# Kernel optimization log

Hardware: AMD Instinct MI355X
Metric: run time of the kernel (lower is better)

The kernel has to match this reference:

```python
import jax, jax.numpy as jnp
import numpy as np

B, T, H, D = 4, 2048, 16, 64
HID = H * D
ROPE_THETA = 10000.0


def _rope_tables(t, d, theta):
    # frequencies over half the head dim, duplicated to full head_dim
    inv_freq = 1.0 / (theta ** (np.arange(0, d, 2, dtype=np.float32) / d))  # (d/2,)
    pos = np.arange(t, dtype=np.float32)
    freqs = np.outer(pos, inv_freq)                      # (T, d/2)
    emb = np.concatenate([freqs, freqs], axis=-1)        # (T, d)
    return jnp.asarray(np.cos(emb)), jnp.asarray(np.sin(emb))


def setup_inputs() -> dict:
    key = jax.random.key(0)
    ks = jax.random.split(key, 5)
    s = 1.0 / np.sqrt(HID)
    cos, sin = _rope_tables(T, D, ROPE_THETA)
    return {
        "x": jax.random.normal(ks[0], (B, T, HID), dtype=jnp.float32),
        "cos": cos,
        "sin": sin,
        "wq": jax.random.normal(ks[1], (HID, HID), dtype=jnp.float32) * s,
        "wk": jax.random.normal(ks[2], (HID, HID), dtype=jnp.float32) * s,
        "wv": jax.random.normal(ks[3], (HID, HID), dtype=jnp.float32) * s,
        "wo": jax.random.normal(ks[4], (HID, HID), dtype=jnp.float32) * s,
    }


def _rotate_half(x):
    x1, x2 = jnp.split(x, 2, axis=-1)
    return jnp.concatenate([-x2, x1], axis=-1)


def reference(x, cos, sin, wq, wk, wv, wo):
    b, t, _ = x.shape
    # QKV projections (nn.Linear: y = x @ W^T), reshape to (B, H, T, D)
    q = (x @ wq.T).reshape(b, t, H, D).transpose(0, 2, 1, 3)
    k = (x @ wk.T).reshape(b, t, H, D).transpose(0, 2, 1, 3)
    v = (x @ wv.T).reshape(b, t, H, D).transpose(0, 2, 1, 3)
    # RoPE
    c = cos[None, None, :, :]
    s = sin[None, None, :, :]
    q = q * c + _rotate_half(q) * s
    k = k * c + _rotate_half(k) * s
    # causal SDPA
    scale = 1.0 / jnp.sqrt(jnp.asarray(D, dtype=x.dtype))
    scores = jnp.einsum("bhqd,bhkd->bhqk", q, k) * scale
    causal = jnp.tril(jnp.ones((t, t), dtype=bool))
    scores = jnp.where(causal[None, None], scores, jnp.finfo(scores.dtype).min)
    attn = jax.nn.softmax(scores, axis=-1)
    out = jnp.einsum("bhqk,bhkd->bhqd", attn, v)
    out = out.transpose(0, 2, 1, 3).reshape(b, t, HID)
    return out @ wo.T
```

## Files before the change

### kernel.cpp

```cpp
#include <hip/hip_runtime.h>

#define BSZ 4
#define TT 2048
#define NH 16
#define HD 64
#define HID 1024
#define BT 8192
#define BH 64

typedef unsigned short u16;
typedef unsigned int u32;
typedef unsigned long long u64;
typedef __attribute__((ext_vector_type(4))) float f32x4;
typedef __attribute__((ext_vector_type(8))) short bf16x8;

#define MFMA32(a, b, c) __builtin_amdgcn_mfma_f32_16x16x32_bf16(a, b, c, 0, 0, 0)

typedef const __attribute__((address_space(1))) u32* gp32;
typedef __attribute__((address_space(3))) u32* lp32;

__device__ __forceinline__ u16 f2bf(float f) {
    union { float f; u32 u; } x; x.f = f;
    u32 r = x.u + 0x7FFFu + ((x.u >> 16) & 1u);
    return (u16)(r >> 16);
}

__device__ __forceinline__ void fexp2x4(f32x4& v) {
    float a = v[0], b = v[1], c = v[2], d = v[3];
    asm("v_exp_f32 %0, %0\n\t"
        "v_exp_f32 %1, %1\n\t"
        "v_exp_f32 %2, %2\n\t"
        "v_exp_f32 %3, %3\n\t"
        "s_nop 1"
        : "+v"(a), "+v"(b), "+v"(c), "+v"(d));
    v[0] = a; v[1] = b; v[2] = c; v[3] = d;
}

__global__ __launch_bounds__(256) void cast_kernel(const float* __restrict__ src,
                                                   u16* __restrict__ dst, int n4) {
    int i = blockIdx.x * 256 + threadIdx.x;
    if (i >= n4) return;
    f32x4 v = *(const f32x4*)(src + (size_t)i * 4);
    uint2 u;
    u.x = (u32)f2bf(v[0]) | ((u32)f2bf(v[1]) << 16);
    u.y = (u32)f2bf(v[2]) | ((u32)f2bf(v[3]) << 16);
    *(uint2*)(dst + (size_t)i * 4) = u;
}

__global__ __launch_bounds__(256)
void cast_w_kernel(const float* __restrict__ wq, const float* __restrict__ wk,
                   const float* __restrict__ wv, const float* __restrict__ wo,
                   u16* __restrict__ wqkv, u16* __restrict__ wo_bf) {
    int g = blockIdx.x >> 10;
    int i = (blockIdx.x & 1023) * 256 + threadIdx.x;
    const float* src = (g == 0) ? wq : (g == 1) ? wk : (g == 2) ? wv : wo;
    u16* dst = (g == 3) ? wo_bf : wqkv + (size_t)g * HID * HID;
    f32x4 v = *(const f32x4*)(src + (size_t)i * 4);
    uint2 u;
    u.x = (u32)f2bf(v[0]) | ((u32)f2bf(v[1]) << 16);
    u.y = (u32)f2bf(v[2]) | ((u32)f2bf(v[3]) << 16);
    *(uint2*)(dst + (size_t)i * 4) = u;
}

template<int MODE>
__global__ __launch_bounds__(512, 2)
void gemm_bt(const u16* __restrict__ A, const u16* __restrict__ W,
             float* __restrict__ Cf, u16* __restrict__ qkv, u16* __restrict__ vt,
             const float* __restrict__ cosT, const float* __restrict__ sinT) {
    __shared__ __align__(16) u16 sh[3 * 24576];
    const int tid  = threadIdx.x;
    const int wid  = tid >> 6, lane = tid & 63;
    const int lrow = lane & 15, lk = lane >> 4;
    const int wm   = (wid >> 1) * 64, wn = (wid & 1) * 64;
    const int xcd  = blockIdx.x & 7;
    const int i_   = blockIdx.x >> 3;
    const int mt   = xcd * 4 + (i_ & 3);
    const int nt   = i_ >> 2;
    const int m0   = mt * 256, n0 = nt * 128;

    auto stageA = [&](int buf, int kk, int half) {
        u16* dst = sh + buf * 24576;
        #pragma unroll
        for (int s = 0; s < 2; ++s) {
            int l16 = half * 1024 + s * 512 + tid;
            int r = l16 >> 3, c = l16 & 7;
            int gc = (c ^ (r & 7)) * 8;
            __builtin_amdgcn_global_load_lds(
                (gp32)&A[(size_t)(m0 + r) * HID + kk + gc],
                (lp32)&dst[l16 * 8], 16, 0, 0);
        }
    };
    auto stageB = [&](int buf, int kk) {
        u16* dst = sh + buf * 24576 + 16384;
        #pragma unroll
        for (int s = 0; s < 2; ++s) {
            int l16 = s * 512 + tid;
            int r = l16 >> 3, c = l16 & 7;
            int gc = (c ^ (r & 7)) * 8;
            __builtin_amdgcn_global_load_lds(
                (gp32)&W[(size_t)(n0 + r) * HID + kk + gc],
                (lp32)&dst[l16 * 8], 16, 0, 0);
        }
    };

    f32x4 acc[4][4] = {};

    stageA(0, 0, 0); stageA(0, 0, 1); stageB(0, 0);
    stageA(1, 64, 0); stageA(1, 64, 1); stageB(1, 64);

    int b = 0;
    for (int t = 0; t < 16; ++t) {
        if (t < 15) asm volatile("s_waitcnt vmcnt(6)" ::: "memory");
        else        asm volatile("s_waitcnt vmcnt(0)" ::: "memory");
        __builtin_amdgcn_s_barrier();
        const u16* As = sh + b * 24576;
        const u16* Bs = As + 16384;
        int b2 = b + 2; if (b2 >= 3) b2 -= 3;

        bf16x8 af[2][4], bfr[2][4];
        #pragma unroll
        for (int h = 0; h < 2; ++h) {
            #pragma unroll
            for (int i = 0; i < 4; ++i) {
                int row = wm + i * 16 + lrow;
                int pc  = (h * 4 + lk) ^ (row & 7);
                af[h][i] = *(const bf16x8*)&As[row * 64 + pc * 8];
            }
            #pragma unroll
            for (int j = 0; j < 4; ++j) {
                int row = wn + j * 16 + lrow;
                int pc  = (h * 4 + lk) ^ (row & 7);
                bfr[h][j] = *(const bf16x8*)&Bs[row * 64 + pc * 8];
            }
        }
        if (t + 2 < 16) {
            const int kk2 = (t + 2) * 64;
            stageA(b2, kk2, 0); stageB(b2, kk2); stageA(b2, kk2, 1);
        }
        __builtin_amdgcn_s_setprio(1);
        #pragma unroll
        for (int h = 0; h < 2; ++h)
            #pragma unroll
            for (int i = 0; i < 4; ++i)
                #pragma unroll
                for (int j = 0; j < 4; ++j)
                    acc[i][j] = MFMA32(af[h][i], bfr[h][j], acc[i][j]);
        __builtin_amdgcn_s_setprio(0);
        ++b; if (b == 3) b = 0;
    }
    __syncthreads();

    if (MODE == 0) {
        const int bb = m0 >> 11, tl0 = m0 & (TT - 1);
        if (nt < 16) {
            const float QSC = (nt < 8) ? 0.125f * 1.44269504f : 1.0f;
            #pragma unroll
            for (int i = 0; i < 4; ++i)
                #pragma unroll
                for (int r = 0; r < 4; ++r) {
                    int tl = (m0 + wm + i * 16 + lk * 4 + r) & (TT - 1);
                    #pragma unroll
                    for (int j = 0; j < 2; ++j) {
                        int dd = j * 16 + lrow;
                        float c = cosT[tl * HD + dd], s = sinT[tl * HD + dd];
                        float v1 = acc[i][j][r], v2 = acc[i][j + 2][r];
                        acc[i][j][r]     = (v1 * c - v2 * s) * QSC;
                        acc[i][j + 2][r] = (v2 * c + v1 * s) * QSC;
                    }
                }
            #pragma unroll
            for (int i = 0; i < 4; ++i)
                #pragma unroll
                for (int j = 0; j < 4; ++j)
                    #pragma unroll
                    for (int r = 0; r < 4; ++r)
                        sh[(wm + i * 16 + lk * 4 + r) * 136 + wn + j * 16 + lrow] =
                            f2bf(acc[i][j][r]);
            __syncthreads();
            #pragma unroll
            for (int p = 0; p < 8; ++p) {
                int idx = p * 512 + tid;
                int r = idx >> 4, c16 = idx & 15;
                f32x4 v = *(const f32x4*)&sh[r * 136 + c16 * 8];
                int nfull = n0 + c16 * 8;
                int proj = nfull >> 10, nl = nfull & 1023;
                int h = nl >> 6, d = nl & 63;
                u16* dst = qkv + (size_t)proj * BT * HID +
                           (((size_t)(bb * NH + h) * TT + tl0 + r) * HD + d);
                *(f32x4*)dst = v;
            }
        } else {
            #pragma unroll
            for (int i = 0; i < 4; ++i)
                #pragma unroll
                for (int j = 0; j < 4; ++j)
                    #pragma unroll
                    for (int r = 0; r < 4; ++r)
                        sh[(wn + j * 16 + lrow) * 272 + wm + i * 16 + lk * 4 + r] =
                            f2bf(acc[i][j][r]);
            __syncthreads();
            #pragma unroll
            for (int p = 0; p < 8; ++p) {
                int oc  = p * 512 + tid;
                int t8  = oc & 31;
                int col = oc >> 5;
                f32x4 v = *(const f32x4*)&sh[col * 272 + t8 * 8];
                int nl = (n0 - 2048) + col;
                int h = nl >> 6, d = nl & 63;
                *(f32x4*)&vt[((size_t)(bb * NH + h) * HD + d) * TT + tl0 + t8 * 8] = v;
            }
        }
    } else {
        #pragma unroll
        for (int i = 0; i < 4; ++i)
            #pragma unroll
            for (int j = 0; j < 4; ++j)
                #pragma unroll
                for (int r = 0; r < 4; ++r) {
                    int m = m0 + wm + i * 16 + lk * 4 + r;
                    int n = n0 + wn + j * 16 + lrow;
                    Cf[(size_t)m * HID + n] = acc[i][j][r];
                }
    }
}

__device__ __forceinline__ u32 cvtpk(float lo, float hi) {
    u32 r;
    asm("v_cvt_pk_bf16_f32 %0, %1, %2" : "=v"(r) : "v"(lo), "v"(hi));
    return r;
}
__device__ __forceinline__ bf16x8 packP(const f32x4& a, const f32x4& b) {
    union { bf16x8 v; u32 w[4]; } u;
    u.w[0] = cvtpk(a[0], a[1]); u.w[1] = cvtpk(a[2], a[3]);
    u.w[2] = cvtpk(b[0], b[1]); u.w[3] = cvtpk(b[2], b[3]);
    return u.v;
}

#define VST 68

__global__ __launch_bounds__(256)
void attn_kernel(const u16* __restrict__ q, const u16* __restrict__ k,
                 const u16* __restrict__ vt, u16* __restrict__ o) {
    __shared__ u16 Ks[64 * 72];
    __shared__ u16 Vts[64 * VST];
    const int tid  = threadIdx.x;
    const int w    = tid >> 6, lane = tid & 63;
    const int lrow = lane & 15, lk = lane >> 4;
    const int nlid = (blockIdx.x & 7) * 128 + (blockIdx.x >> 3);
    const int p    = nlid & 15;
    const int bh   = nlid >> 4;
    const int q0a  = 64 * p, q0b = 64 * (31 - p);
    const size_t hb = (size_t)bh * TT * HD;

    bf16x8 qfa[2], qfb[2];
    #pragma unroll
    for (int kq = 0; kq < 2; ++kq) {
        qfa[kq] = *(const bf16x8*)&q[hb + (size_t)(q0a + w * 16 + lrow) * HD + kq * 32 + lk * 8];
        qfb[kq] = *(const bf16x8*)&q[hb + (size_t)(q0b + w * 16 + lrow) * HD + kq * 32 + lk * 8];
    }

    f32x4 oa[4] = {}, obc[4] = {};
    f32x4 la4 = {}, lb4 = {};

    const int r0 = tid >> 3, f0 = (tid & 7) * 8;
    const int r1 = (tid + 256) >> 3, f1 = (tid & 7) * 8;

    f32x4 pk0 = *(const f32x4*)&k[hb + (size_t)r0 * HD + f0];
    f32x4 pk1 = *(const f32x4*)&k[hb + (size_t)r1 * HD + f1];
    f32x4 pv0 = *(const f32x4*)&vt[hb + (size_t)r0 * TT + f0];
    f32x4 pv1 = *(const f32x4*)&vt[hb + (size_t)r1 * TT + f1];

    const int nIter = 32 - p;
    for (int it = 0; it < nIter; ++it) {
        const bool a_act = (it <= p);
        __syncthreads();
        *(f32x4*)&Ks[r0 * 72 + f0]   = pk0;
        *(f32x4*)&Ks[r1 * 72 + f1]   = pk1;
        *(f32x4*)&Vts[r0 * VST + f0] = pv0;
        *(f32x4*)&Vts[r1 * VST + f1] = pv1;
        __syncthreads();
        if (it + 1 < nIter) {
            const int nn = (it + 1) * 64;
            pk0 = *(const f32x4*)&k[hb + (size_t)(nn + r0) * HD + f0];
            pk1 = *(const f32x4*)&k[hb + (size_t)(nn + r1) * HD + f1];
            pv0 = *(const f32x4*)&vt[hb + (size_t)r0 * TT + nn + f0];
            pv1 = *(const f32x4*)&vt[hb + (size_t)r1 * TT + nn + f1];
        }

        bf16x8 kf0[4], kf1[4];
        #pragma unroll
        for (int mt = 0; mt < 4; ++mt) {
            kf0[mt] = *(const bf16x8*)&Ks[(mt * 16 + lrow) * 72 + lk * 8];
            kf1[mt] = *(const bf16x8*)&Ks[(mt * 16 + lrow) * 72 + 32 + lk * 8];
        }

        {
            f32x4 s[4] = {};
            __builtin_amdgcn_s_setprio(1);
            #pragma unroll
            for (int mt = 0; mt < 4; ++mt) {
                s[mt] = MFMA32(kf0[mt], qfb[0], s[mt]);
                s[mt] = MFMA32(kf1[mt], qfb[1], s[mt]);
            }
            __builtin_amdgcn_s_setprio(0);
            if (it == nIter - 1) {
                #pragma unroll
                for (int mt = 0; mt < 4; ++mt)
                    #pragma unroll
                    for (int r = 0; r < 4; ++r)
                        if (mt * 16 + lk * 4 + r > w * 16 + lrow) s[mt][r] = -1e30f;
            }
            #pragma unroll
            for (int mt = 0; mt < 4; ++mt) {
                fexp2x4(s[mt]);
                lb4 += s[mt];
            }
            bf16x8 p0 = packP(s[0], s[1]), p1 = packP(s[2], s[3]);
            __builtin_amdgcn_s_setprio(1);
            #pragma unroll
            for (int t2 = 0; t2 < 2; ++t2)
                #pragma unroll
                for (int dm = 0; dm < 4; ++dm) {
                    union { bf16x8 v; struct { u64 lo, hi; } u; } vf;
                    const u16* vrow = &Vts[(dm * 16 + lrow) * VST + t2 * 32 + lk * 4];
                    vf.u.lo = *(const u64*)vrow;
                    vf.u.hi = *(const u64*)(vrow + 16);
                    obc[dm] = MFMA32(vf.v, t2 ? p1 : p0, obc[dm]);
                }
            __builtin_amdgcn_s_setprio(0);
        }

        if (a_act) {
            f32x4 s[4] = {};
            __builtin_amdgcn_s_setprio(1);
            #pragma unroll
            for (int mt = 0; mt < 4; ++mt) {
                s[mt] = MFMA32(kf0[mt], qfa[0], s[mt]);
                s[mt] = MFMA32(kf1[mt], qfa[1], s[mt]);
            }
            __builtin_amdgcn_s_setprio(0);
            if (it == p) {
                #pragma unroll
                for (int mt = 0; mt < 4; ++mt)
                    #pragma unroll
                    for (int r = 0; r < 4; ++r)
                        if (mt * 16 + lk * 4 + r > w * 16 + lrow) s[mt][r] = -1e30f;
            }
            #pragma unroll
            for (int mt = 0; mt < 4; ++mt) {
                fexp2x4(s[mt]);
                la4 += s[mt];
            }
            bf16x8 p0 = packP(s[0], s[1]), p1 = packP(s[2], s[3]);
            __builtin_amdgcn_s_setprio(1);
            #pragma unroll
            for (int t2 = 0; t2 < 2; ++t2)
                #pragma unroll
                for (int dm = 0; dm < 4; ++dm) {
                    union { bf16x8 v; struct { u64 lo, hi; } u; } vf;
                    const u16* vrow = &Vts[(dm * 16 + lrow) * VST + t2 * 32 + lk * 4];
                    vf.u.lo = *(const u64*)vrow;
                    vf.u.hi = *(const u64*)(vrow + 16);
                    oa[dm] = MFMA32(vf.v, t2 ? p1 : p0, oa[dm]);
                }
            __builtin_amdgcn_s_setprio(0);
        }
    }

    float lia = la4[0] + la4[1] + la4[2] + la4[3];
    float lib = lb4[0] + lb4[1] + lb4[2] + lb4[3];
    lia += __shfl_xor(lia, 16, 64); lia += __shfl_xor(lia, 32, 64);
    lib += __shfl_xor(lib, 16, 64); lib += __shfl_xor(lib, 32, 64);
    const int b = bh >> 4, h = bh & 15;
    const float inva = 1.f / lia, invb = 1.f / lib;
    #pragma unroll
    for (int dm = 0; dm < 4; ++dm) {
        uint2 pk;
        pk.x = cvtpk(oa[dm][0] * inva, oa[dm][1] * inva);
        pk.y = cvtpk(oa[dm][2] * inva, oa[dm][3] * inva);
        int row = q0a + w * 16 + lrow;
        *(uint2*)&o[((size_t)(b * TT + row)) * HID + h * HD + dm * 16 + lk * 4] = pk;
        pk.x = cvtpk(obc[dm][0] * invb, obc[dm][1] * invb);
        pk.y = cvtpk(obc[dm][2] * invb, obc[dm][3] * invb);
        row = q0b + w * 16 + lrow;
        *(uint2*)&o[((size_t)(b * TT + row)) * HID + h * HD + dm * 16 + lk * 4] = pk;
    }
}

extern "C" void kernel_launch(void* const* d_in, const int* in_sizes, int n_in,
                              void* d_out, int out_size, void* d_ws, size_t ws_size,
                              hipStream_t stream) {
    const float* x    = (const float*)d_in[0];
    const float* cosT = (const float*)d_in[1];
    const float* sinT = (const float*)d_in[2];
    const float* wq   = (const float*)d_in[3];
    const float* wk   = (const float*)d_in[4];
    const float* wv   = (const float*)d_in[5];
    const float* wo   = (const float*)d_in[6];
    float* out = (float*)d_out;

    char* ws = (char*)d_ws;
    size_t off = 0;
    u16* x_bf  = (u16*)(ws + off); off += (size_t)BT * HID * 2;
    u16* wqkv  = (u16*)(ws + off); off += (size_t)3 * HID * HID * 2;
    u16* wo_bf = (u16*)(ws + off); off += (size_t)HID * HID * 2;
    u16* qb    = (u16*)(ws + off); off += (size_t)BT * HID * 2;
    u16* kb    = (u16*)(ws + off); off += (size_t)BT * HID * 2;
    u16* vtb   = (u16*)(ws + off); off += (size_t)BT * HID * 2;
    u16* ob    = (u16*)(ws + off); off += (size_t)BT * HID * 2;
    (void)kb;

    cast_kernel<<<(BT * HID / 4 + 255) / 256, 256, 0, stream>>>(x, x_bf, BT * HID / 4);
    cast_w_kernel<<<4096, 256, 0, stream>>>(wq, wk, wv, wo, wqkv, wo_bf);

    gemm_bt<0><<<dim3(768), 512, 0, stream>>>(
        x_bf, wqkv, nullptr, qb, vtb, cosT, sinT);

    attn_kernel<<<dim3(1024), 256, 0, stream>>>(qb, kb, vtb, ob);

    gemm_bt<1><<<dim3(256), 512, 0, stream>>>(
        ob, wo_bf, out, nullptr, nullptr, nullptr, nullptr);
}
```

Before: 252.4 us.

## Shrink GEMM tiles to 128x128 with double buffering and merge cast kernels

Merges the activation and weight cast kernels into one launch. Replaces the 256x128 GEMM tile (512 threads, triple-buffered LDS with partial vmcnt waits) with a 128x128 tile (256 threads, double buffering) and doubles the grid sizes. The aim is more blocks, smaller LDS per block for better occupancy, and one fewer launch. In exchange, the loop now waits for all outstanding loads each iteration, which weakens load/compute overlap, and the smaller tile lowers data reuse per block.

After: 248.0 us. Within noise of the previous version (-1.7%).

```diff
diff --git a/kernel.cpp b/kernel.cpp
--- a/kernel.cpp
+++ b/kernel.cpp
@@ -36,10 +36,25 @@
     v[0] = a; v[1] = b; v[2] = c; v[3] = d;
 }
 
-__global__ __launch_bounds__(256) void cast_kernel(const float* __restrict__ src,
-                                                   u16* __restrict__ dst, int n4) {
-    int i = blockIdx.x * 256 + threadIdx.x;
-    if (i >= n4) return;
+__global__ __launch_bounds__(256)
+void cast_all_kernel(const float* __restrict__ x,
+                     const float* __restrict__ wq, const float* __restrict__ wk,
+                     const float* __restrict__ wv, const float* __restrict__ wo,
+                     u16* __restrict__ x_bf, u16* __restrict__ wqkv,
+                     u16* __restrict__ wo_bf) {
+    const int blk = blockIdx.x;
+    const float* src;
+    u16* dst;
+    int i;
+    if (blk < 8192) {
+        src = x; dst = x_bf; i = blk * 256 + threadIdx.x;
+    } else {
+        int wb = blk - 8192;
+        int g  = wb >> 10;
+        i = (wb & 1023) * 256 + threadIdx.x;
+        src = (g == 0) ? wq : (g == 1) ? wk : (g == 2) ? wv : wo;
+        dst = (g == 3) ? wo_bf : wqkv + (size_t)g * HID * HID;
+    }
     f32x4 v = *(const f32x4*)(src + (size_t)i * 4);
     uint2 u;
     u.x = (u32)f2bf(v[0]) | ((u32)f2bf(v[1]) << 16);
@@ -47,76 +62,54 @@
     *(uint2*)(dst + (size_t)i * 4) = u;
 }
 
-__global__ __launch_bounds__(256)
-void cast_w_kernel(const float* __restrict__ wq, const float* __restrict__ wk,
-                   const float* __restrict__ wv, const float* __restrict__ wo,
-                   u16* __restrict__ wqkv, u16* __restrict__ wo_bf) {
-    int g = blockIdx.x >> 10;
-    int i = (blockIdx.x & 1023) * 256 + threadIdx.x;
-    const float* src = (g == 0) ? wq : (g == 1) ? wk : (g == 2) ? wv : wo;
-    u16* dst = (g == 3) ? wo_bf : wqkv + (size_t)g * HID * HID;
-    f32x4 v = *(const f32x4*)(src + (size_t)i * 4);
-    uint2 u;
-    u.x = (u32)f2bf(v[0]) | ((u32)f2bf(v[1]) << 16);
-    u.y = (u32)f2bf(v[2]) | ((u32)f2bf(v[3]) << 16);
-    *(uint2*)(dst + (size_t)i * 4) = u;
-}
-
 template<int MODE>
-__global__ __launch_bounds__(512, 2)
+__global__ __launch_bounds__(256, 2)
 void gemm_bt(const u16* __restrict__ A, const u16* __restrict__ W,
              float* __restrict__ Cf, u16* __restrict__ qkv, u16* __restrict__ vt,
              const float* __restrict__ cosT, const float* __restrict__ sinT) {
-    __shared__ __align__(16) u16 sh[3 * 24576];
+    __shared__ __align__(16) u16 sh[2 * 16384];
     const int tid  = threadIdx.x;
     const int wid  = tid >> 6, lane = tid & 63;
     const int lrow = lane & 15, lk = lane >> 4;
     const int wm   = (wid >> 1) * 64, wn = (wid & 1) * 64;
     const int xcd  = blockIdx.x & 7;
     const int i_   = blockIdx.x >> 3;
-    const int mt   = xcd * 4 + (i_ & 3);
-    const int nt   = i_ >> 2;
-    const int m0   = mt * 256, n0 = nt * 128;
-
-    auto stageA = [&](int buf, int kk, int half) {
-        u16* dst = sh + buf * 24576;
-        #pragma unroll
-        for (int s = 0; s < 2; ++s) {
-            int l16 = half * 1024 + s * 512 + tid;
+    const int mt   = xcd * 8 + (i_ & 7);
+    const int nt   = i_ >> 3;
+    const int m0   = mt * 128, n0 = nt * 128;
+
+    auto stage = [&](int slot, int kk) {
+        u16* dstA = sh + slot * 16384;
+        u16* dstB = dstA + 8192;
+        #pragma unroll
+        for (int s = 0; s < 4; ++s) {
+            int l16 = s * 256 + tid;
             int r = l16 >> 3, c = l16 & 7;
             int gc = (c ^ (r & 7)) * 8;
             __builtin_amdgcn_global_load_lds(
                 (gp32)&A[(size_t)(m0 + r) * HID + kk + gc],
-                (lp32)&dst[l16 * 8], 16, 0, 0);
-        }
-    };
-    auto stageB = [&](int buf, int kk) {
-        u16* dst = sh + buf * 24576 + 16384;
-        #pragma unroll
-        for (int s = 0; s < 2; ++s) {
-            int l16 = s * 512 + tid;
+                (lp32)&dstA[l16 * 8], 16, 0, 0);
+        }
+        #pragma unroll
+        for (int s = 0; s < 4; ++s) {
+            int l16 = s * 256 + tid;
             int r = l16 >> 3, c = l16 & 7;
             int gc = (c ^ (r & 7)) * 8;
             __builtin_amdgcn_global_load_lds(
                 (gp32)&W[(size_t)(n0 + r) * HID + kk + gc],
-                (lp32)&dst[l16 * 8], 16, 0, 0);
+                (lp32)&dstB[l16 * 8], 16, 0, 0);
         }
     };
 
     f32x4 acc[4][4] = {};
 
-    stageA(0, 0, 0); stageA(0, 0, 1); stageB(0, 0);
-    stageA(1, 64, 0); stageA(1, 64, 1); stageB(1, 64);
-
-    int b = 0;
+    stage(0, 0);
+
     for (int t = 0; t < 16; ++t) {
-        if (t < 15) asm volatile("s_waitcnt vmcnt(6)" ::: "memory");
-        else        asm volatile("s_waitcnt vmcnt(0)" ::: "memory");
+        asm volatile("s_waitcnt vmcnt(0)" ::: "memory");
         __builtin_amdgcn_s_barrier();
-        const u16* As = sh + b * 24576;
-        const u16* Bs = As + 16384;
-        int b2 = b + 2; if (b2 >= 3) b2 -= 3;
-
+        const u16* As = sh + (t & 1) * 16384;
+        const u16* Bs = As + 8192;
         bf16x8 af[2][4], bfr[2][4];
         #pragma unroll
         for (int h = 0; h < 2; ++h) {
@@ -133,10 +126,7 @@
                 bfr[h][j] = *(const bf16x8*)&Bs[row * 64 + pc * 8];
             }
         }
-        if (t + 2 < 16) {
-            const int kk2 = (t + 2) * 64;
-            stageA(b2, kk2, 0); stageB(b2, kk2); stageA(b2, kk2, 1);
-        }
+        if (t + 1 < 16) stage((t + 1) & 1, (t + 1) * 64);
         __builtin_amdgcn_s_setprio(1);
         #pragma unroll
         for (int h = 0; h < 2; ++h)
@@ -146,7 +136,6 @@
                 for (int j = 0; j < 4; ++j)
                     acc[i][j] = MFMA32(af[h][i], bfr[h][j], acc[i][j]);
         __builtin_amdgcn_s_setprio(0);
-        ++b; if (b == 3) b = 0;
     }
     __syncthreads();
 
@@ -179,7 +168,7 @@
             __syncthreads();
             #pragma unroll
             for (int p = 0; p < 8; ++p) {
-                int idx = p * 512 + tid;
+                int idx = p * 256 + tid;
                 int r = idx >> 4, c16 = idx & 15;
                 f32x4 v = *(const f32x4*)&sh[r * 136 + c16 * 8];
                 int nfull = n0 + c16 * 8;
@@ -196,15 +185,15 @@
                 for (int j = 0; j < 4; ++j)
                     #pragma unroll
                     for (int r = 0; r < 4; ++r)
-                        sh[(wn + j * 16 + lrow) * 272 + wm + i * 16 + lk * 4 + r] =
+                        sh[(wn + j * 16 + lrow) * 136 + wm + i * 16 + lk * 4 + r] =
                             f2bf(acc[i][j][r]);
             __syncthreads();
             #pragma unroll
             for (int p = 0; p < 8; ++p) {
-                int oc  = p * 512 + tid;
-                int t8  = oc & 31;
-                int col = oc >> 5;
-                f32x4 v = *(const f32x4*)&sh[col * 272 + t8 * 8];
+                int oc  = p * 256 + tid;
+                int t8  = oc & 15;
+                int col = oc >> 4;
+                f32x4 v = *(const f32x4*)&sh[col * 136 + t8 * 8];
                 int nl = (n0 - 2048) + col;
                 int h = nl >> 6, d = nl & 63;
                 *(f32x4*)&vt[((size_t)(bb * NH + h) * HD + d) * TT + tl0 + t8 * 8] = v;
@@ -410,14 +399,13 @@
     u16* ob    = (u16*)(ws + off); off += (size_t)BT * HID * 2;
     (void)kb;
 
-    cast_kernel<<<(BT * HID / 4 + 255) / 256, 256, 0, stream>>>(x, x_bf, BT * HID / 4);
-    cast_w_kernel<<<4096, 256, 0, stream>>>(wq, wk, wv, wo, wqkv, wo_bf);
-
-    gemm_bt<0><<<dim3(768), 512, 0, stream>>>(
+    cast_all_kernel<<<12288, 256, 0, stream>>>(x, wq, wk, wv, wo, x_bf, wqkv, wo_bf);
+
+    gemm_bt<0><<<dim3(1536), 256, 0, stream>>>(
         x_bf, wqkv, nullptr, qb, vtb, cosT, sinT);
 
     attn_kernel<<<dim3(1024), 256, 0, stream>>>(qb, kb, vtb, ob);
 
-    gemm_bt<1><<<dim3(256), 512, 0, stream>>>(
+    gemm_bt<1><<<dim3(512), 256, 0, stream>>>(
         ob, wo_bf, out, nullptr, nullptr, nullptr, nullptr);
 }
```
